# Performance work log

Measured on AMD Instinct MI355X. Metric: run time of the kernel, lower is better.

Reference implementation:

```python
import jax, jax.numpy as jnp
import numpy as np

B, M, D = 4096, 200, 100          # batch, max_neighbor, embed_dim
NSYM, NENT = 100001, 5000         # num_symbols+1, num_entities


def setup_inputs() -> dict:
    key = jax.random.key(0)
    ks = jax.random.split(key, 12)
    s = 0.05  # weight init scale to keep activations sane
    return {
        "connections": jax.random.randint(ks[0], (B, M, 3), 0, NENT),
        "target": jax.random.randint(ks[1], (B, 1, 2), 0, NENT),
        "symbol_emb": jax.random.normal(ks[2], (NSYM, D), jnp.float32),
        "co_entities": jax.random.uniform(ks[3], (NENT, NENT), dtype=jnp.float32),
        "gcn_w_weight": jax.random.normal(ks[4], (D, 2 * D), jnp.float32) * s,
        "gcn_w_bias": jax.random.normal(ks[5], (D,), jnp.float32) * s,
        "gcn_b": jnp.zeros((D,), jnp.float32),
        "attn_w_weight": jax.random.normal(ks[6], (1, D), jnp.float32) * s,
        "attn_w_bias": jnp.zeros((1,), jnp.float32),
        "gate_w_weight": jax.random.normal(ks[7], (1, D), jnp.float32) * s,
        "gate_w_bias": jnp.zeros((1,), jnp.float32),
        "gate_b": jnp.zeros((1,), jnp.float32),
    }


def reference(connections, target, symbol_emb, co_entities,
              gcn_w_weight, gcn_w_bias, gcn_b,
              attn_w_weight, attn_w_bias,
              gate_w_weight, gate_w_bias, gate_b):
    # --- neighbor gather ---
    relations = connections[:, :, 1]            # [B, M]
    entities = connections[:, :, 2]             # [B, M]
    entself = connections[:, 0, 0]              # [B]
    rel_embeds = symbol_emb[relations]          # [B, M, D]
    ent_embeds = symbol_emb[entities]           # [B, M, D]
    entself_embeds = symbol_emb[entself]        # [B, D]

    # co-occurrence weights: co[b, m] = co_entities[entities[b,m], target_ent[b]]
    target_ent = target[:, 0, 0]                # [B]
    co_weight = co_entities[entities, target_ent[:, None]]  # [B, M]

    # --- linear + leaky_relu (gcn) ---
    concat = jnp.concatenate([rel_embeds, ent_embeds], axis=-1)   # [B, M, 2D]
    out = jnp.einsum('bmk,dk->bmd', concat, gcn_w_weight) + gcn_w_bias + gcn_b
    out = jax.nn.leaky_relu(out, negative_slope=0.01)             # [B, M, D]

    # --- attention over neighbors ---
    attn_out = jnp.einsum('bmd,od->bmo', out, attn_w_weight) + attn_w_bias  # [B, M, 1]
    attn_weight = jax.nn.softmax(attn_out, axis=1)
    out_attn = jnp.einsum('bmd,bmo->bd', out, attn_weight)        # [B, D]

    # --- sigmoid gate ---
    gate = jax.nn.sigmoid(out_attn @ gate_w_weight.T + gate_w_bias + gate_b)  # [B, 1]
    out_neigh = out_attn * gate

    # --- co-weighted neighbor aggregation ---
    neighbor_emb = jnp.einsum('bm,bmd->bd', co_weight, ent_embeds)  # [B, D]

    return out_neigh + entself_embeds * (1.0 - gate) + neighbor_emb
```

## Files before the change

kernel.cpp:

```cpp
#include <hip/hip_runtime.h>

#define BB   4096
#define MM   200
#define DD   100
#define NENT 5000
#define LPW  27
#define PTW  101

typedef _Float16 f16x2 __attribute__((ext_vector_type(2)));
typedef unsigned uint2v __attribute__((ext_vector_type(2)));

#if defined(__has_builtin)
#if __has_builtin(__builtin_amdgcn_fdot2)
#define HAS_FDOT2 1
#endif
#endif

__device__ __forceinline__ f16x2 uh(unsigned u) { return __builtin_bit_cast(f16x2, u); }
__device__ __forceinline__ float2 h2f(f16x2 h) { return make_float2((float)h.x, (float)h.y); }


__global__ __launch_bounds__(256) void precompute_kernel(
    const float* __restrict__ sym, const float* __restrict__ W,
    const float* __restrict__ wb, const float* __restrict__ gb,
    _Float16* __restrict__ Pr, _Float16* __restrict__ PES)
{
    __shared__ _Float16 Wt[200 * 102];
    const int tid = threadIdx.x;
    for (int j = tid; j < 20000; j += 256) {
        int d = j / 200, k = j % 200;
        Wt[k * 102 + d] = (_Float16)W[j];
    }
    __syncthreads();

    const int i = blockIdx.x * 256 + tid;
    if (i >= NENT * 50) return;
    const int e = i / 50, dp = i % 50;
    const float* se = sym + e * DD;

    float pr0 = 0.f, pr1 = 0.f, pe0 = 0.f, pe1 = 0.f;
    for (int k = 0; k < 100; k++) {
        float a = se[k];
        f16x2 w01 = *(const f16x2*)&Wt[k * 102 + 2 * dp];
        f16x2 w23 = *(const f16x2*)&Wt[(k + 100) * 102 + 2 * dp];
        pr0 = fmaf(a, (float)w01.x, pr0);
        pr1 = fmaf(a, (float)w01.y, pr1);
        pe0 = fmaf(a, (float)w23.x, pe0);
        pe1 = fmaf(a, (float)w23.y, pe1);
    }
    const int d0 = 2 * dp;
    pr0 += wb[d0]     + gb[d0];
    pr1 += wb[d0 + 1] + gb[d0 + 1];

    *(f16x2*)&Pr[e * DD + d0]           = f16x2{(_Float16)pr0, (_Float16)pr1};
    *(f16x2*)&PES[e * 2 * DD + d0]      = f16x2{(_Float16)pe0, (_Float16)pe1};
    *(f16x2*)&PES[e * 2 * DD + DD + d0] = f16x2{(_Float16)se[d0], (_Float16)se[d0 + 1]};
}

__global__ __launch_bounds__(256, 4) void main_kernel(
    const int*  __restrict__ conn, const int* __restrict__ target,
    const float* __restrict__ sym, const float* __restrict__ co,
    const _Float16* __restrict__ Pr, const _Float16* __restrict__ PES,
    const float* __restrict__ attn_w,
    const float* __restrict__ gate_w, const float* __restrict__ gate_wb,
    const float* __restrict__ gate_b,
    float* __restrict__ outp)
{
    __shared__ float    scratch[MM * LPW];
    __shared__ unsigned idx_s[MM];
    __shared__ float    co_s[MM];
    __shared__ float    ev_s[MM];
    __shared__ float    red[8];
    float* lp_s = scratch;
    float* part = scratch;

    const int t = threadIdx.x;
    const int b = blockIdx.x;
    const int* cb = conn + b * (MM * 3);
    const int lane = t & 63, wid = t >> 6;

    if (t < MM) {
        int r = cb[t * 3 + 1];
        int e = cb[t * 3 + 2];
        idx_s[t] = (unsigned)r | ((unsigned)e << 16);
        int tgt = target[b * 2];
        co_s[t] = co[(long)e * NENT + tgt];
    }
    __syncthreads();

    const int g = t / 25, dq = t % 25;
    const bool act = (t < 250);

    float4 awf = *(const float4*)&attn_w[4 * dq];
#ifdef HAS_FDOT2
    f16x2 aw01 = f16x2{(_Float16)awf.x, (_Float16)awf.y};
    f16x2 aw23 = f16x2{(_Float16)awf.z, (_Float16)awf.w};
#endif
    const _Float16 slope = (_Float16)0.01f;

    f16x2 nb01 = f16x2{(_Float16)0.f, (_Float16)0.f};
    f16x2 nb23 = nb01;
    uint2v xs[20];

    if (act) {
        #pragma unroll
        for (int it = 0; it < 20; ++it) {
            int m = g + 10 * it;
            unsigned ir = idx_s[m];
            int r = ir & 0xffff, e = ir >> 16;
            uint2v pru = *(const uint2v*)(Pr + r * DD + 4 * dq);
            uint2v peu = *(const uint2v*)(PES + e * 2 * DD + 4 * dq);
            uint2v syu = *(const uint2v*)(PES + e * 2 * DD + DD + 4 * dq);
            f16x2 x01 = uh(pru.x) + uh(peu.x);
            f16x2 x23 = uh(pru.y) + uh(peu.y);
            x01 = __builtin_elementwise_max(x01, x01 * slope);
            x23 = __builtin_elementwise_max(x23, x23 * slope);
            xs[it].x = __builtin_bit_cast(unsigned, x01);
            xs[it].y = __builtin_bit_cast(unsigned, x23);
            float lp;
#ifdef HAS_FDOT2
            lp = __builtin_amdgcn_fdot2(x01, aw01, 0.0f, false);
            lp = __builtin_amdgcn_fdot2(x23, aw23, lp, false);
#else
            float2 f01 = h2f(x01), f23 = h2f(x23);
            lp = f01.x * awf.x + f01.y * awf.y + f23.x * awf.z + f23.y * awf.w;
#endif
            lp_s[m * LPW + dq] = lp;
            _Float16 coh = (_Float16)co_s[m];
            f16x2 co2 = f16x2{coh, coh};
            nb01 = co2 * uh(syu.x) + nb01;
            nb23 = co2 * uh(syu.y) + nb23;
        }
    }
    __syncthreads();

    float logit = -3.0e38f;
    if (t < MM) {
        const float* row = &lp_s[t * LPW];
        float s0 = (row[0] + row[1]) + (row[2] + row[3]);
        float s1 = (row[4] + row[5]) + (row[6] + row[7]);
        float s2 = (row[8] + row[9]) + (row[10] + row[11]);
        float s3 = (row[12] + row[13]) + (row[14] + row[15]);
        float s4 = (row[16] + row[17]) + (row[18] + row[19]);
        float s5 = (row[20] + row[21]) + (row[22] + row[23]);
        logit = ((s0 + s1) + (s2 + s3)) + ((s4 + s5) + row[24]);
    }

    float v = logit;
    for (int off = 32; off >= 1; off >>= 1) v = fmaxf(v, __shfl_xor(v, off));
    if (lane == 0) red[wid] = v;
    __syncthreads();
    float gmax = fmaxf(fmaxf(red[0], red[1]), fmaxf(red[2], red[3]));
    float ev = (t < MM) ? __expf(logit - gmax) : 0.f;
    if (t < MM) ev_s[t] = ev;
    float s = ev;
    for (int off = 32; off >= 1; off >>= 1) s += __shfl_xor(s, off);
    if (lane == 0) red[4 + wid] = s;
    __syncthreads();
    float gsum = (red[4] + red[5]) + (red[6] + red[7]);

    float oa0 = 0.f, oa1 = 0.f, oa2 = 0.f, oa3 = 0.f;
    if (act) {
        #pragma unroll
        for (int it = 0; it < 20; ++it) {
            int m = g + 10 * it;
            float w = ev_s[m];
            float2 f01 = h2f(uh(xs[it].x));
            float2 f23 = h2f(uh(xs[it].y));
            oa0 = fmaf(w, f01.x, oa0);
            oa1 = fmaf(w, f01.y, oa1);
            oa2 = fmaf(w, f23.x, oa2);
            oa3 = fmaf(w, f23.y, oa3);
        }
    }
    float inv = 1.f / gsum;
    oa0 *= inv; oa1 *= inv; oa2 *= inv; oa3 *= inv;

    if (act) {
        float* po = &part[g * PTW + 4 * dq];
        po[0] = oa0; po[1] = oa1; po[2] = oa2; po[3] = oa3;
        float2 n01 = h2f(nb01), n23 = h2f(nb23);
        float* pn = &part[(10 + g) * PTW + 4 * dq];
        pn[0] = n01.x; pn[1] = n01.y; pn[2] = n23.x; pn[3] = n23.y;
    }
    __syncthreads();

    float oaf = 0.f, nbf = 0.f;
    if (t < DD) {
        #pragma unroll
        for (int g2 = 0; g2 < 10; ++g2) {
            oaf += part[g2 * PTW + t];
            nbf += part[(10 + g2) * PTW + t];
        }
    }

    float p = (t < DD) ? oaf * gate_w[t] : 0.f;
    for (int off = 32; off >= 1; off >>= 1) p += __shfl_xor(p, off);
    if (lane == 0) red[wid] = p;
    __syncthreads();
    float dot = (red[0] + red[1]) + (red[2] + red[3]);
    float gt = 1.f / (1.f + __expf(-(dot + gate_wb[0] + gate_b[0])));

    if (t < DD) {
        float self_v = sym[cb[0] * DD + t];
        outp[b * DD + t] = oaf * gt + self_v * (1.f - gt) + nbf;
    }
}

extern "C" void kernel_launch(void* const* d_in, const int* in_sizes, int n_in,
                              void* d_out, int out_size, void* d_ws, size_t ws_size,
                              hipStream_t stream) {
    const int*   conn    = (const int*)  d_in[0];
    const int*   target  = (const int*)  d_in[1];
    const float* sym     = (const float*)d_in[2];
    const float* co      = (const float*)d_in[3];
    const float* W       = (const float*)d_in[4];
    const float* wb      = (const float*)d_in[5];
    const float* gb      = (const float*)d_in[6];
    const float* attn_w  = (const float*)d_in[7];
    const float* gate_w  = (const float*)d_in[9];
    const float* gate_wb = (const float*)d_in[10];
    const float* gate_b  = (const float*)d_in[11];

    _Float16* Pr  = (_Float16*)d_ws;
    _Float16* PES = (_Float16*)((char*)d_ws + 1000000);

    precompute_kernel<<<(NENT * 50 + 255) / 256, 256, 0, stream>>>(
        sym, W, wb, gb, Pr, PES);

    main_kernel<<<BB, 256, 0, stream>>>(
        conn, target, sym, co, Pr, PES,
        attn_w, gate_w, gate_wb, gate_b, (float*)d_out);
}
```

Baseline: 65.91 us.

## Store logit partials in fp16 and defer neighbor gather for higher occupancy

Per-(m, dq) attention partial logits are now stored in LDS as fp16 with row stride 28, which roughly halves the scratch footprint, and launch bounds ask for 8 blocks per SIMD instead of 4. The co-occurrence load is kept in a register and written to LDS only after the softmax max pass, so its global latency is no longer exposed at the first barrier. The co-weighted symbol gather and accumulation move from the first loop to the second, which lowers live registers in the first loop. In exchange, partial logits lose precision, and the tighter register budget could cause spills.

```diff
diff --git a/kernel.cpp b/kernel.cpp
--- a/kernel.cpp
+++ b/kernel.cpp
@@ -4,7 +4,7 @@
 #define MM   200
 #define DD   100
 #define NENT 5000
-#define LPW  27
+#define LPW  28
 #define PTW  101
 
 typedef _Float16 f16x2 __attribute__((ext_vector_type(2)));
@@ -57,7 +57,7 @@
     *(f16x2*)&PES[e * 2 * DD + DD + d0] = f16x2{(_Float16)se[d0], (_Float16)se[d0 + 1]};
 }
 
-__global__ __launch_bounds__(256, 4) void main_kernel(
+__global__ __launch_bounds__(256, 8) void main_kernel(
     const int*  __restrict__ conn, const int* __restrict__ target,
     const float* __restrict__ sym, const float* __restrict__ co,
     const _Float16* __restrict__ Pr, const _Float16* __restrict__ PES,
@@ -66,25 +66,26 @@
     const float* __restrict__ gate_b,
     float* __restrict__ outp)
 {
-    __shared__ float    scratch[MM * LPW];
+    __shared__ __align__(16) unsigned char scratch_raw[MM * LPW * 2];
     __shared__ unsigned idx_s[MM];
     __shared__ float    co_s[MM];
     __shared__ float    ev_s[MM];
     __shared__ float    red[8];
-    float* lp_s = scratch;
-    float* part = scratch;
+    _Float16* lp_s = (_Float16*)scratch_raw;
+    float*    part = (float*)scratch_raw;
 
     const int t = threadIdx.x;
     const int b = blockIdx.x;
     const int* cb = conn + b * (MM * 3);
     const int lane = t & 63, wid = t >> 6;
 
+    float co_reg = 0.f;
     if (t < MM) {
         int r = cb[t * 3 + 1];
         int e = cb[t * 3 + 2];
         idx_s[t] = (unsigned)r | ((unsigned)e << 16);
         int tgt = target[b * 2];
-        co_s[t] = co[(long)e * NENT + tgt];
+        co_reg = co[(long)e * NENT + tgt];
     }
     __syncthreads();
 
@@ -98,8 +99,6 @@
 #endif
     const _Float16 slope = (_Float16)0.01f;
 
-    f16x2 nb01 = f16x2{(_Float16)0.f, (_Float16)0.f};
-    f16x2 nb23 = nb01;
     uint2v xs[20];
 
     if (act) {
@@ -110,7 +109,6 @@
             int r = ir & 0xffff, e = ir >> 16;
             uint2v pru = *(const uint2v*)(Pr + r * DD + 4 * dq);
             uint2v peu = *(const uint2v*)(PES + e * 2 * DD + 4 * dq);
-            uint2v syu = *(const uint2v*)(PES + e * 2 * DD + DD + 4 * dq);
             f16x2 x01 = uh(pru.x) + uh(peu.x);
             f16x2 x23 = uh(pru.y) + uh(peu.y);
             x01 = __builtin_elementwise_max(x01, x01 * slope);
@@ -125,25 +123,28 @@
             float2 f01 = h2f(x01), f23 = h2f(x23);
             lp = f01.x * awf.x + f01.y * awf.y + f23.x * awf.z + f23.y * awf.w;
 #endif
-            lp_s[m * LPW + dq] = lp;
-            _Float16 coh = (_Float16)co_s[m];
-            f16x2 co2 = f16x2{coh, coh};
-            nb01 = co2 * uh(syu.x) + nb01;
-            nb23 = co2 * uh(syu.y) + nb23;
+            lp_s[m * LPW + dq] = (_Float16)lp;
         }
     }
     __syncthreads();
 
     float logit = -3.0e38f;
     if (t < MM) {
-        const float* row = &lp_s[t * LPW];
-        float s0 = (row[0] + row[1]) + (row[2] + row[3]);
-        float s1 = (row[4] + row[5]) + (row[6] + row[7]);
-        float s2 = (row[8] + row[9]) + (row[10] + row[11]);
-        float s3 = (row[12] + row[13]) + (row[14] + row[15]);
-        float s4 = (row[16] + row[17]) + (row[18] + row[19]);
-        float s5 = (row[20] + row[21]) + (row[22] + row[23]);
-        logit = ((s0 + s1) + (s2 + s3)) + ((s4 + s5) + row[24]);
+        const _Float16* row = lp_s + t * LPW;
+        const unsigned* rw = (const unsigned*)row;
+        float acc0 = 0.f, acc1 = 0.f, acc2 = 0.f, acc3 = 0.f;
+        #pragma unroll
+        for (int i = 0; i < 12; i += 4) {
+            float2 a = h2f(uh(rw[i]));
+            float2 b2 = h2f(uh(rw[i + 1]));
+            float2 c = h2f(uh(rw[i + 2]));
+            float2 d = h2f(uh(rw[i + 3]));
+            acc0 += a.x + a.y;
+            acc1 += b2.x + b2.y;
+            acc2 += c.x + c.y;
+            acc3 += d.x + d.y;
+        }
+        logit = (acc0 + acc1) + (acc2 + acc3) + (float)row[24];
     }
 
     float v = logit;
@@ -152,7 +153,10 @@
     __syncthreads();
     float gmax = fmaxf(fmaxf(red[0], red[1]), fmaxf(red[2], red[3]));
     float ev = (t < MM) ? __expf(logit - gmax) : 0.f;
-    if (t < MM) ev_s[t] = ev;
+    if (t < MM) {
+        ev_s[t] = ev;
+        co_s[t] = co_reg;
+    }
     float s = ev;
     for (int off = 32; off >= 1; off >>= 1) s += __shfl_xor(s, off);
     if (lane == 0) red[4 + wid] = s;
@@ -160,6 +164,8 @@
     float gsum = (red[4] + red[5]) + (red[6] + red[7]);
 
     float oa0 = 0.f, oa1 = 0.f, oa2 = 0.f, oa3 = 0.f;
+    f16x2 nb01 = f16x2{(_Float16)0.f, (_Float16)0.f};
+    f16x2 nb23 = nb01;
     if (act) {
         #pragma unroll
         for (int it = 0; it < 20; ++it) {
@@ -171,6 +177,12 @@
             oa1 = fmaf(w, f01.y, oa1);
             oa2 = fmaf(w, f23.x, oa2);
             oa3 = fmaf(w, f23.y, oa3);
+            int e = idx_s[m] >> 16;
+            uint2v syu = *(const uint2v*)(PES + e * 2 * DD + DD + 4 * dq);
+            _Float16 coh = (_Float16)co_s[m];
+            f16x2 co2 = f16x2{coh, coh};
+            nb01 = co2 * uh(syu.x) + nb01;
+            nb23 = co2 * uh(syu.y) + nb23;
         }
     }
     float inv = 1.f / gsum;
```

New measurement: 81.79 us. 24.1% more time.

## Pad precomputed tables to 128 and use online softmax with quad-per-neighbor gathers

Applied to the files above, without the earlier changes.

Pads the precomputed fp16 tables to 128-wide rows so each neighbor's row can be read with 16-byte vector loads by a quad of four threads. The main kernel no longer stages per-neighbor logits in shared memory. It computes the attention logit per neighbor through quad shuffles, exponentiates without subtracting the max, and accumulates the weighted sums in fp16 registers before doing wave and cross-wave reductions. This drops several block barriers and the shared-memory logit table. In exchange, skipping the max subtraction and accumulating in fp16 risks overflow and lost precision.

```diff
diff --git a/kernel.cpp b/kernel.cpp
--- a/kernel.cpp
+++ b/kernel.cpp
@@ -4,11 +4,9 @@
 #define MM   200
 #define DD   100
 #define NENT 5000
-#define LPW  27
-#define PTW  101
+#define DP   128
 
 typedef _Float16 f16x2 __attribute__((ext_vector_type(2)));
-typedef unsigned uint2v __attribute__((ext_vector_type(2)));
 
 #if defined(__has_builtin)
 #if __has_builtin(__builtin_amdgcn_fdot2)
@@ -17,7 +15,7 @@
 #endif
 
 __device__ __forceinline__ f16x2 uh(unsigned u) { return __builtin_bit_cast(f16x2, u); }
-__device__ __forceinline__ float2 h2f(f16x2 h) { return make_float2((float)h.x, (float)h.y); }
+__device__ __forceinline__ unsigned hu(f16x2 h) { return __builtin_bit_cast(unsigned, h); }
 
 
 __global__ __launch_bounds__(256) void precompute_kernel(
@@ -34,27 +32,33 @@
     __syncthreads();
 
     const int i = blockIdx.x * 256 + tid;
-    if (i >= NENT * 50) return;
-    const int e = i / 50, dp = i % 50;
-    const float* se = sym + e * DD;
-
-    float pr0 = 0.f, pr1 = 0.f, pe0 = 0.f, pe1 = 0.f;
-    for (int k = 0; k < 100; k++) {
-        float a = se[k];
-        f16x2 w01 = *(const f16x2*)&Wt[k * 102 + 2 * dp];
-        f16x2 w23 = *(const f16x2*)&Wt[(k + 100) * 102 + 2 * dp];
-        pr0 = fmaf(a, (float)w01.x, pr0);
-        pr1 = fmaf(a, (float)w01.y, pr1);
-        pe0 = fmaf(a, (float)w23.x, pe0);
-        pe1 = fmaf(a, (float)w23.y, pe1);
-    }
+    if (i >= NENT * 64) return;
+    const int e = i >> 6, dp = i & 63;
     const int d0 = 2 * dp;
-    pr0 += wb[d0]     + gb[d0];
-    pr1 += wb[d0 + 1] + gb[d0 + 1];
-
-    *(f16x2*)&Pr[e * DD + d0]           = f16x2{(_Float16)pr0, (_Float16)pr1};
-    *(f16x2*)&PES[e * 2 * DD + d0]      = f16x2{(_Float16)pe0, (_Float16)pe1};
-    *(f16x2*)&PES[e * 2 * DD + DD + d0] = f16x2{(_Float16)se[d0], (_Float16)se[d0 + 1]};
+
+    if (dp < 50) {
+        const float* se = sym + e * DD;
+        float pr0 = 0.f, pr1 = 0.f, pe0 = 0.f, pe1 = 0.f;
+        for (int k = 0; k < 100; k++) {
+            float a = se[k];
+            f16x2 w01 = *(const f16x2*)&Wt[k * 102 + d0];
+            f16x2 w23 = *(const f16x2*)&Wt[(k + 100) * 102 + d0];
+            pr0 = fmaf(a, (float)w01.x, pr0);
+            pr1 = fmaf(a, (float)w01.y, pr1);
+            pe0 = fmaf(a, (float)w23.x, pe0);
+            pe1 = fmaf(a, (float)w23.y, pe1);
+        }
+        pr0 += wb[d0]     + gb[d0];
+        pr1 += wb[d0 + 1] + gb[d0 + 1];
+        *(f16x2*)&Pr[e * DP + d0]            = f16x2{(_Float16)pr0, (_Float16)pr1};
+        *(f16x2*)&PES[e * 2 * DP + d0]       = f16x2{(_Float16)pe0, (_Float16)pe1};
+        *(f16x2*)&PES[e * 2 * DP + DP + d0]  = f16x2{(_Float16)se[d0], (_Float16)se[d0 + 1]};
+    } else {
+        f16x2 z = f16x2{(_Float16)0.f, (_Float16)0.f};
+        *(f16x2*)&Pr[e * DP + d0]           = z;
+        *(f16x2*)&PES[e * 2 * DP + d0]      = z;
+        *(f16x2*)&PES[e * 2 * DP + DP + d0] = z;
+    }
 }
 
 __global__ __launch_bounds__(256, 4) void main_kernel(
@@ -66,144 +70,141 @@
     const float* __restrict__ gate_b,
     float* __restrict__ outp)
 {
-    __shared__ float    scratch[MM * LPW];
-    __shared__ unsigned idx_s[MM];
-    __shared__ float    co_s[MM];
-    __shared__ float    ev_s[MM];
-    __shared__ float    red[8];
-    float* lp_s = scratch;
-    float* part = scratch;
+    __shared__ unsigned oa_l[4][64];
+    __shared__ unsigned nb_l[4][64];
+    __shared__ float    gs_l[4];
 
     const int t = threadIdx.x;
-    const int b = blockIdx.x;
-    const int* cb = conn + b * (MM * 3);
-    const int lane = t & 63, wid = t >> 6;
-
-    if (t < MM) {
-        int r = cb[t * 3 + 1];
-        int e = cb[t * 3 + 2];
-        idx_s[t] = (unsigned)r | ((unsigned)e << 16);
-        int tgt = target[b * 2];
-        co_s[t] = co[(long)e * NENT + tgt];
+    const int row = blockIdx.x;
+    const int q = t & 3;
+    const int qid = t >> 2;
+    const int w = t >> 6;
+    const int* cb = conn + row * (MM * 3);
+    const int tgt = target[row * 2];
+
+    f16x2 aw_h[16];
+    #pragma unroll
+    for (int j = 0; j < 16; ++j) {
+        int idx = q * 4 + (j & 3) + 16 * (j >> 2);
+        int d0 = 2 * idx;
+        float a0 = (d0 < DD) ? attn_w[d0] : 0.f;
+        float a1 = (d0 + 1 < DD) ? attn_w[d0 + 1] : 0.f;
+        aw_h[j] = f16x2{(_Float16)a0, (_Float16)a1};
+    }
+
+    int rr[4], ee[4];
+    float cov[4];
+    #pragma unroll
+    for (int it = 0; it < 4; ++it) {
+        int m = it * 64 + qid;
+        if (m < MM) {
+            rr[it] = cb[m * 3 + 1];
+            ee[it] = cb[m * 3 + 2];
+            cov[it] = co[(long)ee[it] * NENT + tgt];
+        }
+    }
+
+    const _Float16 slope = (_Float16)0.01f;
+    f16x2 oa[16], nb[16];
+    #pragma unroll
+    for (int j = 0; j < 16; ++j) {
+        oa[j] = f16x2{(_Float16)0.f, (_Float16)0.f};
+        nb[j] = oa[j];
+    }
+    float gsum = 0.f;
+
+    #pragma unroll
+    for (int it = 0; it < 4; ++it) {
+        int m = it * 64 + qid;
+        if (m < MM) {
+            const char* prb = (const char*)Pr + ((long)rr[it] << 8);
+            const char* peb = (const char*)PES + ((long)ee[it] << 9);
+            unsigned xr[16];
+            float lp = 0.f;
+            #pragma unroll
+            for (int i = 0; i < 4; ++i) {
+                uint4 a4 = *(const uint4*)(prb + q * 16 + i * 64);
+                uint4 b4 = *(const uint4*)(peb + q * 16 + i * 64);
+                unsigned av[4] = {a4.x, a4.y, a4.z, a4.w};
+                unsigned bv[4] = {b4.x, b4.y, b4.z, b4.w};
+                #pragma unroll
+                for (int k = 0; k < 4; ++k) {
+                    f16x2 x = uh(av[k]) + uh(bv[k]);
+                    x = __builtin_elementwise_max(x, x * slope);
+                    xr[i * 4 + k] = hu(x);
+#ifdef HAS_FDOT2
+                    lp = __builtin_amdgcn_fdot2(x, aw_h[i * 4 + k], lp, false);
+#else
+                    lp += (float)x.x * (float)aw_h[i * 4 + k].x
+                        + (float)x.y * (float)aw_h[i * 4 + k].y;
+#endif
+                }
+            }
+            lp += __shfl_xor(lp, 1);
+            lp += __shfl_xor(lp, 2);
+            float ev = __expf(lp);
+            gsum += ev;
+            f16x2 evh = f16x2{(_Float16)ev, (_Float16)ev};
+            f16x2 coh = f16x2{(_Float16)cov[it], (_Float16)cov[it]};
+            #pragma unroll
+            for (int i = 0; i < 4; ++i) {
+                uint4 s4 = *(const uint4*)(peb + 256 + q * 16 + i * 64);
+                unsigned sv[4] = {s4.x, s4.y, s4.z, s4.w};
+                #pragma unroll
+                for (int k = 0; k < 4; ++k) {
+                    int j = i * 4 + k;
+                    oa[j] = evh * uh(xr[j]) + oa[j];
+                    nb[j] = coh * uh(sv[k]) + nb[j];
+                }
+            }
+        }
+    }
+
+    #pragma unroll
+    for (int st = 4; st <= 32; st <<= 1) {
+        gsum += __shfl_xor(gsum, st);
+        #pragma unroll
+        for (int j = 0; j < 16; ++j) {
+            oa[j] = oa[j] + uh((unsigned)__shfl_xor((int)hu(oa[j]), st));
+            nb[j] = nb[j] + uh((unsigned)__shfl_xor((int)hu(nb[j]), st));
+        }
+    }
+    if ((t & 63) < 4) {
+        #pragma unroll
+        for (int j = 0; j < 16; ++j) {
+            int idx = q * 4 + (j & 3) + 16 * (j >> 2);
+            oa_l[w][idx] = hu(oa[j]);
+            nb_l[w][idx] = hu(nb[j]);
+        }
+        if (q == 0) gs_l[w] = gsum;
     }
     __syncthreads();
 
-    const int g = t / 25, dq = t % 25;
-    const bool act = (t < 250);
-
-    float4 awf = *(const float4*)&attn_w[4 * dq];
-#ifdef HAS_FDOT2
-    f16x2 aw01 = f16x2{(_Float16)awf.x, (_Float16)awf.y};
-    f16x2 aw23 = f16x2{(_Float16)awf.z, (_Float16)awf.w};
-#endif
-    const _Float16 slope = (_Float16)0.01f;
-
-    f16x2 nb01 = f16x2{(_Float16)0.f, (_Float16)0.f};
-    f16x2 nb23 = nb01;
-    uint2v xs[20];
-
-    if (act) {
+    if (t < 64) {
+        f16x2 oau = uh(oa_l[0][t]) + uh(oa_l[1][t]);
+        oau = oau + uh(oa_l[2][t]);
+        oau = oau + uh(oa_l[3][t]);
+        f16x2 nbu = uh(nb_l[0][t]) + uh(nb_l[1][t]);
+        nbu = nbu + uh(nb_l[2][t]);
+        nbu = nbu + uh(nb_l[3][t]);
+        float gst = (gs_l[0] + gs_l[1]) + (gs_l[2] + gs_l[3]);
+        float inv = 1.f / gst;
+        float o0 = (float)oau.x * inv, o1 = (float)oau.y * inv;
+        float n0 = (float)nbu.x,       n1 = (float)nbu.y;
+        const int d0 = 2 * t;
+
+        float p = (t < DD / 2) ? o0 * gate_w[d0] + o1 * gate_w[d0 + 1] : 0.f;
         #pragma unroll
-        for (int it = 0; it < 20; ++it) {
-            int m = g + 10 * it;
-            unsigned ir = idx_s[m];
-            int r = ir & 0xffff, e = ir >> 16;
-            uint2v pru = *(const uint2v*)(Pr + r * DD + 4 * dq);
-            uint2v peu = *(const uint2v*)(PES + e * 2 * DD + 4 * dq);
-            uint2v syu = *(const uint2v*)(PES + e * 2 * DD + DD + 4 * dq);
-            f16x2 x01 = uh(pru.x) + uh(peu.x);
-            f16x2 x23 = uh(pru.y) + uh(peu.y);
-            x01 = __builtin_elementwise_max(x01, x01 * slope);
-            x23 = __builtin_elementwise_max(x23, x23 * slope);
-            xs[it].x = __builtin_bit_cast(unsigned, x01);
-            xs[it].y = __builtin_bit_cast(unsigned, x23);
-            float lp;
-#ifdef HAS_FDOT2
-            lp = __builtin_amdgcn_fdot2(x01, aw01, 0.0f, false);
-            lp = __builtin_amdgcn_fdot2(x23, aw23, lp, false);
-#else
-            float2 f01 = h2f(x01), f23 = h2f(x23);
-            lp = f01.x * awf.x + f01.y * awf.y + f23.x * awf.z + f23.y * awf.w;
-#endif
-            lp_s[m * LPW + dq] = lp;
-            _Float16 coh = (_Float16)co_s[m];
-            f16x2 co2 = f16x2{coh, coh};
-            nb01 = co2 * uh(syu.x) + nb01;
-            nb23 = co2 * uh(syu.y) + nb23;
-        }
-    }
-    __syncthreads();
-
-    float logit = -3.0e38f;
-    if (t < MM) {
-        const float* row = &lp_s[t * LPW];
-        float s0 = (row[0] + row[1]) + (row[2] + row[3]);
-        float s1 = (row[4] + row[5]) + (row[6] + row[7]);
-        float s2 = (row[8] + row[9]) + (row[10] + row[11]);
-        float s3 = (row[12] + row[13]) + (row[14] + row[15]);
-        float s4 = (row[16] + row[17]) + (row[18] + row[19]);
-        float s5 = (row[20] + row[21]) + (row[22] + row[23]);
-        logit = ((s0 + s1) + (s2 + s3)) + ((s4 + s5) + row[24]);
-    }
-
-    float v = logit;
-    for (int off = 32; off >= 1; off >>= 1) v = fmaxf(v, __shfl_xor(v, off));
-    if (lane == 0) red[wid] = v;
-    __syncthreads();
-    float gmax = fmaxf(fmaxf(red[0], red[1]), fmaxf(red[2], red[3]));
-    float ev = (t < MM) ? __expf(logit - gmax) : 0.f;
-    if (t < MM) ev_s[t] = ev;
-    float s = ev;
-    for (int off = 32; off >= 1; off >>= 1) s += __shfl_xor(s, off);
-    if (lane == 0) red[4 + wid] = s;
-    __syncthreads();
-    float gsum = (red[4] + red[5]) + (red[6] + red[7]);
-
-    float oa0 = 0.f, oa1 = 0.f, oa2 = 0.f, oa3 = 0.f;
-    if (act) {
-        #pragma unroll
-        for (int it = 0; it < 20; ++it) {
-            int m = g + 10 * it;
-            float w = ev_s[m];
-            float2 f01 = h2f(uh(xs[it].x));
-            float2 f23 = h2f(uh(xs[it].y));
-            oa0 = fmaf(w, f01.x, oa0);
-            oa1 = fmaf(w, f01.y, oa1);
-            oa2 = fmaf(w, f23.x, oa2);
-            oa3 = fmaf(w, f23.y, oa3);
-        }
-    }
-    float inv = 1.f / gsum;
-    oa0 *= inv; oa1 *= inv; oa2 *= inv; oa3 *= inv;
-
-    if (act) {
-        float* po = &part[g * PTW + 4 * dq];
-        po[0] = oa0; po[1] = oa1; po[2] = oa2; po[3] = oa3;
-        float2 n01 = h2f(nb01), n23 = h2f(nb23);
-        float* pn = &part[(10 + g) * PTW + 4 * dq];
-        pn[0] = n01.x; pn[1] = n01.y; pn[2] = n23.x; pn[3] = n23.y;
-    }
-    __syncthreads();
-
-    float oaf = 0.f, nbf = 0.f;
-    if (t < DD) {
-        #pragma unroll
-        for (int g2 = 0; g2 < 10; ++g2) {
-            oaf += part[g2 * PTW + t];
-            nbf += part[(10 + g2) * PTW + t];
-        }
-    }
-
-    float p = (t < DD) ? oaf * gate_w[t] : 0.f;
-    for (int off = 32; off >= 1; off >>= 1) p += __shfl_xor(p, off);
-    if (lane == 0) red[wid] = p;
-    __syncthreads();
-    float dot = (red[0] + red[1]) + (red[2] + red[3]);
-    float gt = 1.f / (1.f + __expf(-(dot + gate_wb[0] + gate_b[0])));
-
-    if (t < DD) {
-        float self_v = sym[cb[0] * DD + t];
-        outp[b * DD + t] = oaf * gt + self_v * (1.f - gt) + nbf;
+        for (int off = 32; off >= 1; off >>= 1) p += __shfl_xor(p, off);
+        float gt = 1.f / (1.f + __expf(-(p + gate_wb[0] + gate_b[0])));
+
+        if (t < DD / 2) {
+            int s_self = cb[0];
+            const float* sv = sym + (long)s_self * DD + d0;
+            float* op = outp + (long)row * DD + d0;
+            op[0] = o0 * gt + sv[0] * (1.f - gt) + n0;
+            op[1] = o1 * gt + sv[1] * (1.f - gt) + n1;
+        }
     }
 }
 
@@ -223,9 +224,9 @@
     const float* gate_b  = (const float*)d_in[11];
 
     _Float16* Pr  = (_Float16*)d_ws;
-    _Float16* PES = (_Float16*)((char*)d_ws + 1000000);
-
-    precompute_kernel<<<(NENT * 50 + 255) / 256, 256, 0, stream>>>(
+    _Float16* PES = (_Float16*)((char*)d_ws + 1280000);
+
+    precompute_kernel<<<(NENT * 64 + 255) / 256, 256, 0, stream>>>(
         sym, W, wb, gb, Pr, PES);
 
     main_kernel<<<BB, 256, 0, stream>>>(
```

Measured after the change: 83.01 us. 1.26x slower.
